# Kernel optimization log

Hardware: AMD Instinct MI355X
Metric: run time of the kernel (lower is better)

The kernel has to match this reference:

```python
import jax, jax.numpy as jnp
import numpy as np

BATCH, LENGTH = 4, 512
D_MODEL, D_STATE, EXPAND = 128, 256, 2
D_INNER = EXPAND * D_MODEL  # 256 (== D_STATE, required by the original broadcasting)


def setup_inputs() -> dict:
    key = jax.random.key(0)
    ks = jax.random.split(key, 8)
    x = jax.random.normal(ks[0], (BATCH, LENGTH, D_MODEL), jnp.float32)
    # bias-free Dense kernels, fan-in scaled; W_delta and A kept small so
    # exp(delta*A)^L stays numerically tame over L=512 steps.
    W_in = jax.random.normal(ks[1], (D_MODEL, 2 * D_INNER), jnp.float32) / np.float32(np.sqrt(D_MODEL))
    W_delta = jax.random.normal(ks[2], (D_INNER, D_INNER), jnp.float32) * np.float32(0.005)
    W_B = jax.random.normal(ks[3], (D_INNER, D_STATE), jnp.float32) / np.float32(np.sqrt(D_INNER))
    W_C = jax.random.normal(ks[4], (D_INNER, D_INNER), jnp.float32) / np.float32(np.sqrt(D_INNER))
    W_out = jax.random.normal(ks[5], (D_INNER, D_MODEL), jnp.float32) / np.float32(np.sqrt(D_INNER))
    A = jax.random.normal(ks[6], (D_INNER, D_STATE), jnp.float32) * np.float32(0.02)
    D = jnp.ones((D_INNER,), jnp.float32)  # unused by the original scan, kept for faithfulness
    return dict(x=x, W_in=W_in, W_delta=W_delta, W_B=W_B, W_C=W_C, W_out=W_out, A=A, D=D)


def reference(x, W_in, W_delta, W_B, W_C, W_out, A, D):
    # in_proj + split
    x_proj = x @ W_in                      # (b, l, 2*d_inner)
    xs, z = jnp.split(x_proj, 2, axis=-1)  # each (b, l, d_inner)
    delta = xs @ W_delta                   # (b, l, d_inner)
    Bv = xs @ W_B                          # (b, l, d_state)
    Cv = xs @ W_C                          # (b, l, d_inner)

    # discretized transition/input, exactly as the original einsums
    deltaA = jnp.exp(jnp.einsum('bld,dn->bldn', delta, A))   # (b, l, d_inner, d_state)
    deltaB = jnp.einsum('bld,bln->bldn', delta, Bv)          # (b, l, d_inner, d_state)

    def step(state, inp):
        dA_i, dB_i, x_i, C_i = inp
        # state: (b, d_inner, d_state); x broadcast over the middle axis as in tf.expand_dims(x,1)
        state = dA_i * state + dB_i * x_i[:, None, :]
        y = jnp.einsum('bdn,bn->bd', state, C_i)
        return state, y

    init = jnp.zeros((x.shape[0], D_INNER, D_STATE), xs.dtype)
    inps = (
        jnp.moveaxis(deltaA, 1, 0),  # (l, b, d, n)
        jnp.moveaxis(deltaB, 1, 0),
        jnp.moveaxis(xs, 1, 0),      # (l, b, d)
        jnp.moveaxis(Cv, 1, 0),
    )
    _, ys = jax.lax.scan(step, init, inps)   # ys: (l, b, d_inner)
    y = jnp.moveaxis(ys, 0, 1)               # (b, l, d_inner)

    y = y * jax.nn.silu(z)
    return y @ W_out                          # (b, l, d_model)
```

## Files before the change

kernel.cpp:

```cpp
#include <hip/hip_runtime.h>
#include <hip/hip_bf16.h>


#define MROWS 2048
#define DM 128
#define DI 256
#define DS 256
#define LLEN 512
#define LC 64
#define NC 8

#define LOG2E 1.44269504088896340736f

typedef short bf16x8 __attribute__((ext_vector_type(8)));
typedef float f32x4  __attribute__((ext_vector_type(4)));
typedef float f32x2  __attribute__((ext_vector_type(2)));

#define FMA2(a, b, c) __builtin_elementwise_fma((a), (b), (c))

__device__ __forceinline__ short f2bf(float f) {
    union { float f; unsigned u; } v; v.f = f;
    unsigned r = v.u + 0x7FFFu + ((v.u >> 16) & 1u);
    return (short)(r >> 16);
}

__device__ __forceinline__ void tconv(float (*tile)[33],
                                      const float* __restrict__ src,
                                      short* __restrict__ dst,
                                      int Ms, int Ns, int ti, int tj, int tid)
{
    const int r = tid >> 5, c = tid & 31;
#pragma unroll
    for (int i = 0; i < 4; ++i)
        tile[r + 8 * i][c] = src[(size_t)(ti * 32 + r + 8 * i) * Ns + tj * 32 + c];
    __syncthreads();
#pragma unroll
    for (int i = 0; i < 4; ++i)
        dst[(size_t)(tj * 32 + r + 8 * i) * Ms + ti * 32 + c] = f2bf(tile[c][r + 8 * i]);
}

__global__ __launch_bounds__(256) void k_proj_mfma(
    const float* __restrict__ x, const float* __restrict__ W_in,
    const float* __restrict__ Wd, const float* __restrict__ Wb,
    const float* __restrict__ Wc, const float* __restrict__ W_out,
    float* __restrict__ xs, short* __restrict__ xs_bf, float* __restrict__ sz,
    short* __restrict__ WdbcT, short* __restrict__ W_outT)
{
    const int t = threadIdx.x;

    if (blockIdx.x >= 8) {
        __shared__ float tile[32][33];
        const int uu = (blockIdx.x - 8) * 32 + blockIdx.y;
        if (uu < 64)       tconv(tile, Wd,    WdbcT,                       256, 256, uu & 7,         uu >> 3,         t);
        else if (uu < 128) tconv(tile, Wb,    WdbcT + (size_t)256 * 256,   256, 256, (uu - 64) & 7,  (uu - 64) >> 3,  t);
        else if (uu < 192) tconv(tile, Wc,    WdbcT + (size_t)512 * 256,   256, 256, (uu - 128) & 7, (uu - 128) >> 3, t);
        else if (uu < 224) tconv(tile, W_out, W_outT,                      256, 128, (uu - 192) & 7, (uu - 192) >> 3, t);
        return;
    }

    __shared__ short As[64][136];
    __shared__ short Bs[64][136];
    f32x4 acc[4] = {};
    const int w = t >> 6, lane = t & 63;
    const int srow = t >> 2, sseg = t & 3;
    const int frow = lane & 15, fk = (lane >> 4) << 3;
    const int r0 = blockIdx.y * 64, n0 = blockIdx.x * 64;

    {
        const float* ap = x + (size_t)(r0 + srow) * DM + sseg * 32;
        short tmp[32];
#pragma unroll
        for (int j = 0; j < 8; ++j) {
            float4 f = *(const float4*)(ap + j * 4);
            tmp[j * 4 + 0] = f2bf(f.x); tmp[j * 4 + 1] = f2bf(f.y);
            tmp[j * 4 + 2] = f2bf(f.z); tmp[j * 4 + 3] = f2bf(f.w);
        }
#pragma unroll
        for (int m = 0; m < 4; ++m)
            *(bf16x8*)&As[srow][sseg * 32 + m * 8] = *(bf16x8*)&tmp[m * 8];
    }
    {
#pragma unroll
        for (int i = 0; i < 32; i += 2) {
            const int k = sseg * 32 + i;
            float f0 = W_in[(size_t)k * 512 + n0 + srow];
            float f1 = W_in[(size_t)(k + 1) * 512 + n0 + srow];
            unsigned pk = (unsigned short)f2bf(f0) | ((unsigned)(unsigned short)f2bf(f1) << 16);
            *(unsigned*)&Bs[srow][k] = pk;
        }
    }
    __syncthreads();

#pragma unroll
    for (int kk = 0; kk < 128; kk += 32) {
        bf16x8 af = *(const bf16x8*)&As[w * 16 + frow][kk + fk];
#pragma unroll
        for (int ct = 0; ct < 4; ++ct) {
            bf16x8 bfr = *(const bf16x8*)&Bs[ct * 16 + frow][kk + fk];
            acc[ct] = __builtin_amdgcn_mfma_f32_16x16x32_bf16(af, bfr, acc[ct], 0, 0, 0);
        }
    }

    const int rr = r0 + w * 16 + (lane >> 4) * 4;
    const int c0 = n0 + (lane & 15);
#pragma unroll
    for (int ct = 0; ct < 4; ++ct) {
        const int c = c0 + ct * 16;
#pragma unroll
        for (int rg = 0; rg < 4; ++rg) {
            const float v = acc[ct][rg];
            const int r = rr + rg;
            if (c < DI) {
                xs[(size_t)r * DI + c]    = v;
                xs_bf[(size_t)r * DI + c] = f2bf(v);
            } else {
                sz[(size_t)r * DI + (c - DI)] = v / (1.f + __expf(-v));
            }
        }
    }
}

__global__ __launch_bounds__(512) void k_dbc(
    const short* __restrict__ xs_bf, const short* __restrict__ WdbcT,
    const float* __restrict__ xs,
    float* __restrict__ dlt, float* __restrict__ u, float* __restrict__ cvv)
{
    __shared__ short As[64][72], Bs[128][72];
    const int blk = blockIdx.x, t = threadIdx.x;
    const int w8 = t >> 6, lane = t & 63;
    const int rf = w8 & 3, ch = w8 >> 2;
    const int frow = lane & 15, fk = (lane >> 4) << 3;
    const int bx = blk % 6, by = blk / 6;
    const int r0 = by * 64, n0 = bx * 128;
    const int arow = t >> 3, ak = (t & 7) * 8;
    const int brow = t >> 2, bk = (t & 3) * 16;
    f32x4 acc[4] = {};

    for (int k0 = 0; k0 < DI; k0 += 64) {
        bf16x8 a0 = *(const bf16x8*)(xs_bf + (size_t)(r0 + arow) * DI + k0 + ak);
        bf16x8 b0 = *(const bf16x8*)(WdbcT + (size_t)(n0 + brow) * DI + k0 + bk);
        bf16x8 b1 = *(const bf16x8*)(WdbcT + (size_t)(n0 + brow) * DI + k0 + bk + 8);
        __syncthreads();
        *(bf16x8*)&As[arow][ak]     = a0;
        *(bf16x8*)&Bs[brow][bk]     = b0;
        *(bf16x8*)&Bs[brow][bk + 8] = b1;
        __syncthreads();
#pragma unroll
        for (int kk = 0; kk < 64; kk += 32) {
            bf16x8 af = *(const bf16x8*)&As[rf * 16 + frow][kk + fk];
#pragma unroll
            for (int ct = 0; ct < 4; ++ct) {
                bf16x8 bfr = *(const bf16x8*)&Bs[(ch * 4 + ct) * 16 + frow][kk + fk];
                acc[ct] = __builtin_amdgcn_mfma_f32_16x16x32_bf16(af, bfr, acc[ct], 0, 0, 0);
            }
        }
    }

    const int rr = r0 + rf * 16 + (lane >> 4) * 4;
    const int nbase = n0 + ch * 64;
    const int wsel = nbase >> 8;
    const int nb = nbase & 255;
#pragma unroll
    for (int ct = 0; ct < 4; ++ct) {
        const int c = nb + ct * 16 + (lane & 15);
#pragma unroll
        for (int rg = 0; rg < 4; ++rg) {
            const float v = acc[ct][rg];
            const size_t idx = (size_t)(rr + rg) * DI + c;
            if (wsel == 0)      dlt[idx] = v;
            else if (wsel == 1) u[idx]   = v * xs[idx];
            else                cvv[idx] = v;
        }
    }
}

__global__ __launch_bounds__(256) void k_scan1(
    const float* __restrict__ dlt, const float* __restrict__ u,
    const float* __restrict__ Aa,
    float* __restrict__ tc, float* __restrict__ dsm)
{
    const int lane = threadIdx.x & 63;
    const int w    = threadIdx.x >> 6;
    const int blk  = blockIdx.x;
    const int b  = blk & 3;
    const int r  = blk >> 2;
    const int c  = r % 7;
    const int d0 = ((r / 7) * 4 + w) * 4;

    __shared__ float4 dls4[4][LC];
    const size_t base = (size_t)b * LLEN * DI + (size_t)c * LC * DI;

    float4 dv = *(const float4*)(dlt + base + (size_t)lane * DI + d0);
    dls4[w][lane] = dv;
    float dsv[4] = { dv.x, dv.y, dv.z, dv.w };
#pragma unroll
    for (int dd = 0; dd < 4; ++dd) {
#pragma unroll
        for (int off = 32; off > 0; off >>= 1)
            dsv[dd] += __shfl_xor(dsv[dd], off);
    }

    const f32x2 one2 = {1.f, 1.f};
    f32x2 c1a[4], c1b[4], c2a[4], c2b[4];
#pragma unroll
    for (int dd = 0; dd < 4; ++dd) {
        float4 a = *(const float4*)(Aa + (size_t)(d0 + dd) * DS + lane * 4);
        c1a[dd] = (f32x2){a.x, a.y};
        c1b[dd] = (f32x2){a.z, a.w};
        c2a[dd] = (f32x2){0.5f * a.x * a.x, 0.5f * a.y * a.y};
        c2b[dd] = (f32x2){0.5f * a.z * a.z, 0.5f * a.w * a.w};
    }

    const float4* up = (const float4*)(u + base) + lane;
    f32x2 s0[4] = {}, s1[4] = {};
    float4 uA[4], uB[4];

#define S1_PRE(UB, G)                                                         \
    {                                                                         \
        _Pragma("unroll")                                                     \
        for (int i = 0; i < 4; ++i)                                           \
            UB[i] = up[(size_t)((G) * 4 + i) * 64];                           \
    }

#define S1_COMP(UB, G)                                                        \
    {                                                                         \
        _Pragma("unroll")                                                     \
        for (int i = 0; i < 4; ++i) {                                         \
            const float4 d4 = dls4[w][(G) * 4 + i];                           \
            const float dla[4] = { d4.x, d4.y, d4.z, d4.w };                  \
            const f32x2 u01 = (f32x2){UB[i].x, UB[i].y};                      \
            const f32x2 u23 = (f32x2){UB[i].z, UB[i].w};                      \
            _Pragma("unroll")                                                 \
            for (int dd = 0; dd < 4; ++dd) {                                  \
                const f32x2 dl2 = (f32x2){dla[dd], dla[dd]};                  \
                f32x2 e0 = FMA2(c2a[dd], dl2, c1a[dd]); e0 = FMA2(e0, dl2, one2); \
                f32x2 e1 = FMA2(c2b[dd], dl2, c1b[dd]); e1 = FMA2(e1, dl2, one2); \
                s0[dd] = FMA2(e0, s0[dd], dl2 * u01);                         \
                s1[dd] = FMA2(e1, s1[dd], dl2 * u23);                         \
            }                                                                 \
        }                                                                     \
    }

    S1_PRE(uA, 0)
    for (int g2 = 0; g2 < 8; ++g2) {
        S1_PRE(uB, g2 * 2 + 1)
        S1_COMP(uA, g2 * 2)
        if (g2 < 7) S1_PRE(uA, g2 * 2 + 2)
        S1_COMP(uB, g2 * 2 + 1)
    }
#undef S1_PRE
#undef S1_COMP

    const size_t rbb = ((size_t)(b * 256 + d0)) * NC + c;
#pragma unroll
    for (int dd = 0; dd < 4; ++dd) {
        *(float4*)(tc + (rbb + (size_t)dd * NC) * 256 + lane * 4) =
            make_float4(s0[dd][0], s0[dd][1], s1[dd][0], s1[dd][1]);
        if (lane == 0) dsm[rbb + dd * NC] = dsv[dd];
    }
}

__global__ __launch_bounds__(256) void k_scan3(
    const float* __restrict__ dlt, const float* __restrict__ u,
    const float* __restrict__ cvv, const float* __restrict__ Aa,
    const float* __restrict__ tc, const float* __restrict__ dsm,
    float* __restrict__ yv)
{
    const int lane = threadIdx.x & 63;
    const int w    = threadIdx.x >> 6;
    const int blk  = blockIdx.x;
    const int b  = blk & 3;
    const int c  = (blk >> 2) & 7;
    const int d0 = ((blk >> 5) * 4 + w) * 4;

    __shared__ float4 dls4[4][LC];
    __shared__ float T[4][LC][17];

    const size_t base = (size_t)b * LLEN * DI + (size_t)c * LC * DI;

    float4 dv = *(const float4*)(dlt + base + (size_t)lane * DI + d0);
    dls4[w][lane] = dv;

    const f32x2 one2 = {1.f, 1.f};
    f32x2 c1a[4], c1b[4], c2a[4], c2b[4];
#pragma unroll
    for (int dd = 0; dd < 4; ++dd) {
        float4 a = *(const float4*)(Aa + (size_t)(d0 + dd) * DS + lane * 4);
        c1a[dd] = (f32x2){a.x, a.y};
        c1b[dd] = (f32x2){a.z, a.w};
        c2a[dd] = (f32x2){0.5f * a.x * a.x, 0.5f * a.y * a.y};
        c2b[dd] = (f32x2){0.5f * a.z * a.z, 0.5f * a.w * a.w};
    }

    f32x2 s0[4] = {}, s1[4] = {};
    for (int cc = 0; cc < c; ++cc) {
#pragma unroll
        for (int dd = 0; dd < 4; ++dd) {
            const size_t rbd = ((size_t)(b * 256 + d0 + dd)) * NC + cc;
            const float4 Tt = *(const float4*)(tc + rbd * 256 + lane * 4);
            const float  Dc = dsm[rbd] * LOG2E;
            s0[dd][0] = exp2f(c1a[dd][0] * Dc) * s0[dd][0] + Tt.x;
            s0[dd][1] = exp2f(c1a[dd][1] * Dc) * s0[dd][1] + Tt.y;
            s1[dd][0] = exp2f(c1b[dd][0] * Dc) * s1[dd][0] + Tt.z;
            s1[dd][1] = exp2f(c1b[dd][1] * Dc) * s1[dd][1] + Tt.w;
        }
    }

    const float4* up = (const float4*)(u + base) + lane;
    const float4* cp = (const float4*)(cvv + base) + lane;
    float* yb = yv + base;

    const int col = lane & 15, seg = lane >> 4;
    float4 uA[4], cA[4], uB[4], cB[4];

#define S3_PRE(UB, CB, G)                                                     \
    {                                                                         \
        _Pragma("unroll")                                                     \
        for (int i = 0; i < 4; ++i) {                                         \
            UB[i] = up[(size_t)((G) * 4 + i) * 64];                           \
            CB[i] = cp[(size_t)((G) * 4 + i) * 64];                           \
        }                                                                     \
    }

#define S3_COMP(UB, CB, G)                                                    \
    {                                                                         \
        _Pragma("unroll")                                                     \
        for (int i = 0; i < 4; ++i) {                                         \
            const float4 d4 = dls4[w][(G) * 4 + i];                           \
            const float dla[4] = { d4.x, d4.y, d4.z, d4.w };                  \
            const f32x2 u01 = (f32x2){UB[i].x, UB[i].y};                      \
            const f32x2 u23 = (f32x2){UB[i].z, UB[i].w};                      \
            const f32x2 c01 = (f32x2){CB[i].x, CB[i].y};                      \
            const f32x2 c23 = (f32x2){CB[i].z, CB[i].w};                      \
            _Pragma("unroll")                                                 \
            for (int dd = 0; dd < 4; ++dd) {                                  \
                const f32x2 dl2 = (f32x2){dla[dd], dla[dd]};                  \
                f32x2 e0 = FMA2(c2a[dd], dl2, c1a[dd]); e0 = FMA2(e0, dl2, one2); \
                f32x2 e1 = FMA2(c2b[dd], dl2, c1b[dd]); e1 = FMA2(e1, dl2, one2); \
                s0[dd] = FMA2(e0, s0[dd], dl2 * u01);                         \
                s1[dd] = FMA2(e1, s1[dd], dl2 * u23);                         \
                f32x2 q = s0[dd] * c01;                                       \
                q = FMA2(s1[dd], c23, q);                                     \
                T[w][lane][dd * 4 + i] = q[0] + q[1];                         \
            }                                                                 \
        }                                                                     \
        float sm = 0.f;                                                       \
        _Pragma("unroll")                                                     \
        for (int rr2 = 0; rr2 < 16; ++rr2)                                    \
            sm += T[w][seg * 16 + rr2][col];                                  \
        sm += __shfl_xor(sm, 16);                                             \
        sm += __shfl_xor(sm, 32);                                             \
        if (lane < 16)                                                        \
            yb[(size_t)((G) * 4 + (col & 3)) * DI + d0 + (col >> 2)] = sm;    \
    }

    S3_PRE(uA, cA, 0)
    for (int g2 = 0; g2 < 8; ++g2) {
        S3_PRE(uB, cB, g2 * 2 + 1)
        S3_COMP(uA, cA, g2 * 2)
        if (g2 < 7) S3_PRE(uA, cA, g2 * 2 + 2)
        S3_COMP(uB, cB, g2 * 2 + 1)
    }
#undef S3_PRE
#undef S3_COMP
}

__global__ __launch_bounds__(256) void k_out_mfma(
    const float* __restrict__ y, const float* __restrict__ szp,
    const short* __restrict__ W_outT, float* __restrict__ out)
{
    __shared__ short As[64][72], Bs[64][72];
    f32x4 acc[4] = {};
    const int tid  = threadIdx.x;
    const int w    = tid >> 6, lane = tid & 63;
    const int srow = tid >> 2, sseg = tid & 3;
    const int frow = lane & 15, fk = (lane >> 4) << 3;
    const int r0 = blockIdx.y * 64, n0 = blockIdx.x * 64;

    for (int k0 = 0; k0 < DI; k0 += 64) {
        const size_t aoff = (size_t)(r0 + srow) * DI + k0 + sseg * 16;
        float4 y0 = *(const float4*)(y + aoff);
        float4 y1 = *(const float4*)(y + aoff + 4);
        float4 y2 = *(const float4*)(y + aoff + 8);
        float4 y3 = *(const float4*)(y + aoff + 12);
        float4 s0 = *(const float4*)(szp + aoff);
        float4 s1 = *(const float4*)(szp + aoff + 4);
        float4 s2 = *(const float4*)(szp + aoff + 8);
        float4 s3 = *(const float4*)(szp + aoff + 12);
        const short* bg = W_outT + (size_t)(n0 + srow) * DI + k0 + sseg * 16;
        bf16x8 b0 = *(const bf16x8*)bg;
        bf16x8 b1 = *(const bf16x8*)(bg + 8);
        bf16x8 a0, a1;
        a0[0] = f2bf(y0.x * s0.x); a0[1] = f2bf(y0.y * s0.y);
        a0[2] = f2bf(y0.z * s0.z); a0[3] = f2bf(y0.w * s0.w);
        a0[4] = f2bf(y1.x * s1.x); a0[5] = f2bf(y1.y * s1.y);
        a0[6] = f2bf(y1.z * s1.z); a0[7] = f2bf(y1.w * s1.w);
        a1[0] = f2bf(y2.x * s2.x); a1[1] = f2bf(y2.y * s2.y);
        a1[2] = f2bf(y2.z * s2.z); a1[3] = f2bf(y2.w * s2.w);
        a1[4] = f2bf(y3.x * s3.x); a1[5] = f2bf(y3.y * s3.y);
        a1[6] = f2bf(y3.z * s3.z); a1[7] = f2bf(y3.w * s3.w);
        __syncthreads();
        *(bf16x8*)&As[srow][sseg * 16]     = a0;
        *(bf16x8*)&As[srow][sseg * 16 + 8] = a1;
        *(bf16x8*)&Bs[srow][sseg * 16]     = b0;
        *(bf16x8*)&Bs[srow][sseg * 16 + 8] = b1;
        __syncthreads();
#pragma unroll
        for (int kk = 0; kk < 64; kk += 32) {
            bf16x8 af = *(const bf16x8*)&As[w * 16 + frow][kk + fk];
#pragma unroll
            for (int ct = 0; ct < 4; ++ct) {
                bf16x8 bfr = *(const bf16x8*)&Bs[ct * 16 + frow][kk + fk];
                acc[ct] = __builtin_amdgcn_mfma_f32_16x16x32_bf16(af, bfr, acc[ct], 0, 0, 0);
            }
        }
    }

    const int rr = r0 + w * 16 + (lane >> 4) * 4;
    const int c0 = n0 + (lane & 15);
#pragma unroll
    for (int ct = 0; ct < 4; ++ct) {
        const int c = c0 + ct * 16;
#pragma unroll
        for (int rg = 0; rg < 4; ++rg)
            out[(size_t)(rr + rg) * DM + c] = acc[ct][rg];
    }
}

extern "C" void kernel_launch(void* const* d_in, const int* in_sizes, int n_in,
                              void* d_out, int out_size, void* d_ws, size_t ws_size,
                              hipStream_t stream)
{
    const float* x       = (const float*)d_in[0];
    const float* W_in    = (const float*)d_in[1];
    const float* W_delta = (const float*)d_in[2];
    const float* W_B     = (const float*)d_in[3];
    const float* W_C     = (const float*)d_in[4];
    const float* W_out   = (const float*)d_in[5];
    const float* A       = (const float*)d_in[6];

    float* out = (float*)d_out;
    float* ws  = (float*)d_ws;

    const size_t S = (size_t)MROWS * DI;
    float* xs  = ws;
    float* sz  = ws + S;
    float* dlt = ws + 2 * S;
    float* u   = ws + 3 * S;
    float* cv  = ws + 4 * S;
    float* yv  = ws + 5 * S;
    float* tc  = ws + 6 * S;
    float* dsm = tc + (size_t)1024 * NC * 256;

    short* xs_bf  = (short*)(dsm + (size_t)1024 * NC);
    short* WdbcT  = xs_bf + (size_t)MROWS * DI;
    short* W_outT = WdbcT + (size_t)768 * DI;

    k_proj_mfma<<<dim3(15, 32), 256, 0, stream>>>(x, W_in, W_delta, W_B, W_C, W_out,
                                                  xs, xs_bf, sz, WdbcT, W_outT);
    k_dbc      <<<dim3(192), 512, 0, stream>>>(xs_bf, WdbcT, xs, dlt, u, cv);
    k_scan1    <<<dim3(448), 256, 0, stream>>>(dlt, u, A, tc, dsm);
    k_scan3    <<<dim3(512), 256, 0, stream>>>(dlt, u, cv, A, tc, dsm, yv);
    k_out_mfma <<<dim3(2, 32), 256, 0, stream>>>(yv, sz, W_outT, out);
}
```

Baseline: 68.98 us.

## Remap block indices so each XCD keeps the same batch and chunk rows across kernels

Block indices in k_dbc, k_scan1, k_scan3 and k_out_mfma are remapped so the low three bits (the XCD a block is dispatched to under round-robin) pick a fixed batch and chunk-parity. Each XCD then produces and consumes the same row ranges of dlt, u, cv and y across consecutive kernels. The aim is to have intermediates hit in that XCD's L2 instead of coming back through the slower shared level. k_scan1 now launches 512 blocks and computes the final chunk's carry, which no later step uses, so it does some extra work to keep the mapping uniform.

```diff
diff --git a/kernel.cpp b/kernel.cpp
--- a/kernel.cpp
+++ b/kernel.cpp
@@ -130,8 +130,11 @@
     const int w8 = t >> 6, lane = t & 63;
     const int rf = w8 & 3, ch = w8 >> 2;
     const int frow = lane & 15, fk = (lane >> 4) << 3;
-    const int bx = blk % 6, by = blk / 6;
-    const int r0 = by * 64, n0 = bx * 128;
+    const int xk = blk & 7, m = blk >> 3;
+    const int b  = xk & 3;
+    const int c  = (xk >> 2) + 2 * (m / 6);
+    const int bx = m % 6;
+    const int r0 = b * 512 + c * 64, n0 = bx * 128;
     const int arow = t >> 3, ak = (t & 7) * 8;
     const int brow = t >> 2, bk = (t & 3) * 16;
     f32x4 acc[4] = {};
@@ -162,11 +165,11 @@
     const int nb = nbase & 255;
 #pragma unroll
     for (int ct = 0; ct < 4; ++ct) {
-        const int c = nb + ct * 16 + (lane & 15);
+        const int cc = nb + ct * 16 + (lane & 15);
 #pragma unroll
         for (int rg = 0; rg < 4; ++rg) {
             const float v = acc[ct][rg];
-            const size_t idx = (size_t)(rr + rg) * DI + c;
+            const size_t idx = (size_t)(rr + rg) * DI + cc;
             if (wsel == 0)      dlt[idx] = v;
             else if (wsel == 1) u[idx]   = v * xs[idx];
             else                cvv[idx] = v;
@@ -182,10 +185,10 @@
     const int lane = threadIdx.x & 63;
     const int w    = threadIdx.x >> 6;
     const int blk  = blockIdx.x;
-    const int b  = blk & 3;
-    const int r  = blk >> 2;
-    const int c  = r % 7;
-    const int d0 = ((r / 7) * 4 + w) * 4;
+    const int xk = blk & 7, g = blk >> 3;
+    const int b  = xk & 3;
+    const int c  = (xk >> 2) + 2 * (g >> 4);
+    const int d0 = (g & 15) * 16 + w * 4;
 
     __shared__ float4 dls4[4][LC];
     const size_t base = (size_t)b * LLEN * DI + (size_t)c * LC * DI;
@@ -269,9 +272,10 @@
     const int lane = threadIdx.x & 63;
     const int w    = threadIdx.x >> 6;
     const int blk  = blockIdx.x;
-    const int b  = blk & 3;
-    const int c  = (blk >> 2) & 7;
-    const int d0 = ((blk >> 5) * 4 + w) * 4;
+    const int xk = blk & 7, g = blk >> 3;
+    const int b  = xk & 3;
+    const int c  = (xk >> 2) + 2 * (g >> 4);
+    const int d0 = (g & 15) * 16 + w * 4;
 
     __shared__ float4 dls4[4][LC];
     __shared__ float T[4][LC][17];
@@ -372,10 +376,15 @@
     __shared__ short As[64][72], Bs[64][72];
     f32x4 acc[4] = {};
     const int tid  = threadIdx.x;
+    const int blk  = blockIdx.x;
     const int w    = tid >> 6, lane = tid & 63;
     const int srow = tid >> 2, sseg = tid & 3;
     const int frow = lane & 15, fk = (lane >> 4) << 3;
-    const int r0 = blockIdx.y * 64, n0 = blockIdx.x * 64;
+    const int xk = blk & 7, m = blk >> 3;
+    const int b  = xk & 3;
+    const int c  = (xk >> 2) + 2 * (m >> 1);
+    const int r0 = b * 512 + c * 64;
+    const int n0 = (m & 1) * 64;
 
     for (int k0 = 0; k0 < DI; k0 += 64) {
         const size_t aoff = (size_t)(r0 + srow) * DI + k0 + sseg * 16;
@@ -420,10 +429,10 @@
     const int c0 = n0 + (lane & 15);
 #pragma unroll
     for (int ct = 0; ct < 4; ++ct) {
-        const int c = c0 + ct * 16;
+        const int cc = c0 + ct * 16;
 #pragma unroll
         for (int rg = 0; rg < 4; ++rg)
-            out[(size_t)(rr + rg) * DM + c] = acc[ct][rg];
+            out[(size_t)(rr + rg) * DM + cc] = acc[ct][rg];
     }
 }
 
@@ -459,7 +468,7 @@
     k_proj_mfma<<<dim3(15, 32), 256, 0, stream>>>(x, W_in, W_delta, W_B, W_C, W_out,
                                                   xs, xs_bf, sz, WdbcT, W_outT);
     k_dbc      <<<dim3(192), 512, 0, stream>>>(xs_bf, WdbcT, xs, dlt, u, cv);
-    k_scan1    <<<dim3(448), 256, 0, stream>>>(dlt, u, A, tc, dsm);
+    k_scan1    <<<dim3(512), 256, 0, stream>>>(dlt, u, A, tc, dsm);
     k_scan3    <<<dim3(512), 256, 0, stream>>>(dlt, u, cv, A, tc, dsm, yv);
-    k_out_mfma <<<dim3(2, 32), 256, 0, stream>>>(yv, sz, W_outT, out);
-}
+    k_out_mfma <<<dim3(64), 256, 0, stream>>>(yv, sz, W_outT, out);
+}
```

New measurement: 65.84 us, median of 2. 4.5% less time.
